# Kernel optimization log

Measured on AMD Instinct MI355X. Metric: run time of the kernel, lower is better.

The kernel has to match this reference:

```python
import jax, jax.numpy as jnp
import numpy as np

N_NODES = 50000
N_EDGES = 800000
IN_C, HID_C, OUT_C = 128, 128, 64
N_GRAPHS = 64
NEG_SLOPE = 0.2


def setup_inputs() -> dict:
    key = jax.random.key(0)
    ks = jax.random.split(key, 16)
    x = jax.random.normal(ks[0], (N_NODES, IN_C), dtype=jnp.float32)
    edge_index = jax.random.randint(ks[1], (2, N_EDGES), 0, N_NODES, dtype=jnp.int64)
    batch = jnp.sort(jax.random.randint(ks[2], (N_NODES,), 0, N_GRAPHS, dtype=jnp.int64))
    dims = [(IN_C, HID_C), (HID_C, HID_C), (HID_C, OUT_C)]
    inp = {"x": x, "edge_index": edge_index, "batch": batch}
    for l, (din, dout) in enumerate(dims):
        s = 1.0 / np.sqrt(din)
        inp[f"W{l}"] = jax.random.normal(ks[3 + 4 * l], (din, dout), dtype=jnp.float32) * s
        inp[f"as{l}"] = jax.random.normal(ks[4 + 4 * l], (dout,), dtype=jnp.float32) * 0.1
        inp[f"ad{l}"] = jax.random.normal(ks[5 + 4 * l], (dout,), dtype=jnp.float32) * 0.1
        inp[f"b{l}"] = jnp.zeros((dout,), dtype=jnp.float32)
    return inp


def gat_conv(x, src, dst, W, a_src, a_dst, b, n_nodes):
    # h: [N, dout]
    h = x @ W
    alpha_src = h @ a_src  # [N]
    alpha_dst = h @ a_dst  # [N]
    logits = jax.nn.leaky_relu(alpha_src[src] + alpha_dst[dst], NEG_SLOPE)  # [E]
    # segment softmax over incoming edges of each dst node
    m = jax.ops.segment_max(logits, dst, num_segments=n_nodes)
    e = jnp.exp(logits - m[dst])
    denom = jax.ops.segment_sum(e, dst, num_segments=n_nodes)
    alpha = e / denom[dst]  # [E]
    out = jax.ops.segment_sum(alpha[:, None] * h[src], dst, num_segments=n_nodes)
    return out + b


def reference(x, edge_index, batch, W0, as0, ad0, b0, W1, as1, ad1, b1, W2, as2, ad2, b2):
    n = x.shape[0]
    # add self loops (PyG GATConv default)
    loop = jnp.arange(n, dtype=edge_index.dtype)
    src = jnp.concatenate([edge_index[0], loop])
    dst = jnp.concatenate([edge_index[1], loop])
    h = jax.nn.relu(gat_conv(x, src, dst, W0, as0, ad0, b0, n))
    h = jax.nn.relu(gat_conv(h, src, dst, W1, as1, ad1, b1, n))
    h = gat_conv(h, src, dst, W2, as2, ad2, b2, n)
    # global_add_pool
    return jax.ops.segment_sum(h, batch, num_segments=N_GRAPHS)
```

## Files before the change

### kernel.cpp

```cpp
#include <hip/hip_runtime.h>
#include <hip/hip_fp16.h>
#include <math.h>

#define N_NODES 50000
#define N_EDGES 800000
#define N_GRAPHS 64
#define NEG_SLOPE 0.2f
#define SLOTS 64

#define BIN_NODES 256
#define NBINS 196
#define CAP 6144
#define P1_BLOCKS 192
#define BATCH 2048

typedef _Float16 f16x8 __attribute__((ext_vector_type(8)));
typedef float f32x4 __attribute__((ext_vector_type(4)));

__device__ __forceinline__ float leaky(float x) {
    return x > 0.f ? x : NEG_SLOPE * x;
}

struct __align__(16) half8 {
    __half2 h[4];
};

__global__ __launch_bounds__(256) void prep_kernel(const float* __restrict__ W0,
                                                   const float* __restrict__ W1,
                                                   const float* __restrict__ W2,
                                                   _Float16* __restrict__ Wt0,
                                                   _Float16* __restrict__ Wt1,
                                                   _Float16* __restrict__ Wt2,
                                                   unsigned int* __restrict__ bin_cursor,
                                                   float* __restrict__ dout, int osz) {
    const int t = blockIdx.x * 256 + threadIdx.x;
    if (t < NBINS) bin_cursor[t] = 0;
    if (t < osz) dout[t] = 0.f;
    const float* W;
    _Float16* Wt;
    int g, CTl, DOUTl;
    if (t < 2048) { W = W0; Wt = Wt0; g = t; CTl = 8; DOUTl = 128; }
    else if (t < 4096) { W = W1; Wt = Wt1; g = t - 2048; CTl = 8; DOUTl = 128; }
    else if (t < 5120) { W = W2; Wt = Wt2; g = t - 4096; CTl = 4; DOUTl = 64; }
    else return;
    const int kt = g / (CTl * 64);
    const int rem = g % (CTl * 64);
    const int ct = rem / 64;
    const int lane = rem % 64;
    const int kbase = kt * 32 + (lane >> 4) * 8;
    const int c = ct * 16 + (lane & 15);
#pragma unroll
    for (int b = 0; b < 8; ++b)
        Wt[(size_t)g * 8 + b] = (_Float16)W[(size_t)(kbase + b) * DOUTl + c];
}

template <int DOUT, typename XT>
__device__ __forceinline__ void mfma_gemm_body(const XT* __restrict__ X,
                                               const _Float16* __restrict__ Wt,
                                               const float* __restrict__ a_src,
                                               const float* __restrict__ a_dst,
                                               _Float16* __restrict__ H,
                                               float* __restrict__ as_,
                                               float* __restrict__ ad_, int N, int bid,
                                               _Float16* xs) {
    constexpr int CT = DOUT / 16;
    const int tid = threadIdx.x;
    const int n0 = bid * 64;

    if constexpr (sizeof(XT) == 4) {
        const float4* X4 = reinterpret_cast<const float4*>(X);
        for (int idx = tid; idx < 64 * 16; idx += 256) {
            const int r = idx >> 4, q = idx & 15;
            const int n = n0 + r;
            float4 v0 = make_float4(0.f, 0.f, 0.f, 0.f), v1 = v0;
            if (n < N) {
                v0 = X4[(size_t)n * 32 + 2 * q];
                v1 = X4[(size_t)n * 32 + 2 * q + 1];
            }
            f16x8 hv;
            hv[0] = (_Float16)v0.x; hv[1] = (_Float16)v0.y;
            hv[2] = (_Float16)v0.z; hv[3] = (_Float16)v0.w;
            hv[4] = (_Float16)v1.x; hv[5] = (_Float16)v1.y;
            hv[6] = (_Float16)v1.z; hv[7] = (_Float16)v1.w;
            *reinterpret_cast<f16x8*>(&xs[r * 128 + ((q ^ (r & 15)) << 3)]) = hv;
        }
    } else {
        const f16x8* X8 = reinterpret_cast<const f16x8*>(X);
        for (int idx = tid; idx < 64 * 16; idx += 256) {
            const int r = idx >> 4, q = idx & 15;
            const int n = n0 + r;
            f16x8 hv = {};
            if (n < N) hv = X8[(size_t)n * 16 + q];
            *reinterpret_cast<f16x8*>(&xs[r * 128 + ((q ^ (r & 15)) << 3)]) = hv;
        }
    }
    __syncthreads();

    const int wave = tid >> 6, lane = tid & 63;
    const int colb = lane & 15;
    const int kg = lane >> 4;
    const int arow = wave * 16 + colb;

    f32x4 acc[CT];
#pragma unroll
    for (int ct = 0; ct < CT; ++ct) {
        acc[ct][0] = 0.f; acc[ct][1] = 0.f; acc[ct][2] = 0.f; acc[ct][3] = 0.f;
    }
    const f16x8* Wt8 = reinterpret_cast<const f16x8*>(Wt);
#pragma unroll
    for (int kt = 0; kt < 4; ++kt) {
        f16x8 A = *reinterpret_cast<const f16x8*>(
            &xs[arow * 128 + (((kt * 4 + kg) ^ (arow & 15)) << 3)]);
#pragma unroll
        for (int ct = 0; ct < CT; ++ct) {
            f16x8 B = Wt8[(kt * CT + ct) * 64 + lane];
            acc[ct] = __builtin_amdgcn_mfma_f32_16x16x32_f16(A, B, acc[ct], 0, 0, 0);
        }
    }

    float ps[4] = {0.f, 0.f, 0.f, 0.f}, pd[4] = {0.f, 0.f, 0.f, 0.f};
#pragma unroll
    for (int ct = 0; ct < CT; ++ct) {
        const int col = ct * 16 + colb;
        const float asv = a_src[col];
        const float adv = a_dst[col];
#pragma unroll
        for (int r = 0; r < 4; ++r) {
            const float d = acc[ct][r];
            ps[r] += d * asv;
            pd[r] += d * adv;
            const int row = n0 + wave * 16 + kg * 4 + r;
            if (row < N) H[(size_t)row * DOUT + col] = (_Float16)d;
        }
    }
#pragma unroll
    for (int off = 1; off < 16; off <<= 1) {
#pragma unroll
        for (int r = 0; r < 4; ++r) {
            ps[r] += __shfl_xor(ps[r], off, 64);
            pd[r] += __shfl_xor(pd[r], off, 64);
        }
    }
    if (colb == 0) {
#pragma unroll
        for (int r = 0; r < 4; ++r) {
            const int row = n0 + wave * 16 + kg * 4 + r;
            if (row < N) {
                as_[row] = ps[r];
                ad_[row] = pd[r];
            }
        }
    }
}

template <int DOUT, typename XT>
__global__ __launch_bounds__(256) void mfma_gemm_kernel(const XT* __restrict__ X,
                                                        const _Float16* __restrict__ Wt,
                                                        const float* __restrict__ a_src,
                                                        const float* __restrict__ a_dst,
                                                        _Float16* __restrict__ H,
                                                        float* __restrict__ as_,
                                                        float* __restrict__ ad_, int N) {
    __shared__ __align__(16) _Float16 xs[64 * 128];
    mfma_gemm_body<DOUT, XT>(X, Wt, a_src, a_dst, H, as_, ad_, N, blockIdx.x, xs);
}

struct P1Smem {
    unsigned int stage[BATCH];
    int hist[NBINS];
    int off[NBINS];
    unsigned int gbase[NBINS];
    int total;
};

__device__ __forceinline__ void fill_pass1(const int* __restrict__ src,
                                           const int* __restrict__ dst,
                                           unsigned int* __restrict__ bin_cursor,
                                           unsigned int* __restrict__ bin_buf,
                                           int E, int bid, void* smem_raw) {
    P1Smem& S = *reinterpret_cast<P1Smem*>(smem_raw);
    const int tid = threadIdx.x;
    const int nbatch = (E + BATCH - 1) / BATCH;
    for (int b = bid; b < nbatch; b += P1_BLOCKS) {
        __syncthreads();
        for (int i = tid; i < NBINS; i += 256) S.hist[i] = 0;
        const int e0 = b * BATCH;
        unsigned int pk[8];
        int rk[8];
        bool ok[8];
#pragma unroll
        for (int k = 0; k < 8; ++k) {
            int e = e0 + tid + k * 256;
            ok[k] = (e < E);
            int d = ok[k] ? dst[e] : 0;
            int s = ok[k] ? src[e] : 0;
            pk[k] = ((unsigned)d << 16) | (unsigned)s;
            rk[k] = 0;
        }
        __syncthreads();
#pragma unroll
        for (int k = 0; k < 8; ++k)
            if (ok[k]) rk[k] = atomicAdd(&S.hist[pk[k] >> 24], 1);
        __syncthreads();
        for (int i = tid; i < NBINS; i += 256) S.off[i] = S.hist[i];
        __syncthreads();
#pragma unroll
        for (int d = 1; d < 256; d <<= 1) {
            int v = 0;
            if (tid < NBINS && tid >= d) v = S.off[tid - d];
            __syncthreads();
            if (tid < NBINS) S.off[tid] += v;
            __syncthreads();
        }
        if (tid == NBINS - 1) S.total = S.off[NBINS - 1];
        __syncthreads();
        if (tid < NBINS) S.off[tid] -= S.hist[tid];
        __syncthreads();
        if (tid < NBINS && S.hist[tid] > 0)
            S.gbase[tid] = atomicAdd(&bin_cursor[tid], (unsigned)S.hist[tid]);
#pragma unroll
        for (int k = 0; k < 8; ++k)
            if (ok[k]) S.stage[S.off[pk[k] >> 24] + rk[k]] = pk[k];
        __syncthreads();
        const int tot = S.total;
        for (int i = tid; i < tot; i += 256) {
            unsigned int v = S.stage[i];
            int bn = v >> 24;
            unsigned int p = S.gbase[bn] + (unsigned)(i - S.off[bn]);
            if (p < CAP) bin_buf[(size_t)bn * CAP + p] = v;
        }
    }
}

__global__ __launch_bounds__(256) void gemm0_fill_kernel(
    const float* __restrict__ X, const _Float16* __restrict__ Wt0,
    const float* __restrict__ a_src, const float* __restrict__ a_dst,
    _Float16* __restrict__ H, float* __restrict__ as_, float* __restrict__ ad_, int N,
    const int* __restrict__ src, const int* __restrict__ dst,
    unsigned int* __restrict__ bin_cursor, unsigned int* __restrict__ bin_buf, int E) {
    __shared__ __align__(16) unsigned char smem[16384];
    if (blockIdx.x < P1_BLOCKS) {
        fill_pass1(src, dst, bin_cursor, bin_buf, E, blockIdx.x, smem);
        return;
    }
    mfma_gemm_body<128, float>(X, Wt0, a_src, a_dst, H, as_, ad_, N, blockIdx.x - P1_BLOCKS,
                               reinterpret_cast<_Float16*>(smem));
}

__global__ __launch_bounds__(256) void fill_pass2(const unsigned int* __restrict__ bin_cursor,
                                                  const unsigned int* __restrict__ bin_buf,
                                                  int* __restrict__ cursor,
                                                  unsigned short* __restrict__ col, int N) {
    __shared__ unsigned short bk[BIN_NODES][SLOTS];
    __shared__ int cnt[BIN_NODES];
    const int b = blockIdx.x;
    const int tid = threadIdx.x;
    const int base = b * BIN_NODES;
    const int nn = min(BIN_NODES, N - base);
    if (nn <= 0) return;
    cnt[tid] = 0;
    __syncthreads();
    const int ec = min((int)bin_cursor[b], CAP);
    for (int i = tid; i < ec; i += 256) {
        unsigned int v = bin_buf[(size_t)b * CAP + i];
        int d = (int)(v >> 16) - base;
        int p = atomicAdd(&cnt[d], 1);
        if (p < SLOTS) bk[d][p] = (unsigned short)(v & 0xFFFFu);
    }
    __syncthreads();
    unsigned int* col32 = reinterpret_cast<unsigned int*>(col);
    const unsigned int* lds32 = reinterpret_cast<const unsigned int*>(&bk[0][0]);
    const int words = nn * (SLOTS / 2);
    for (int i = tid; i < words; i += 256)
        col32[(size_t)base * (SLOTS / 2) + i] = lds32[i];
    if (tid < nn) cursor[base + tid] = cnt[tid];
}

template <int DOUT, bool POOL>
__global__ __launch_bounds__(256) void gather_kernel(const half8* __restrict__ H8,
                                                     const float* __restrict__ as_,
                                                     const float* __restrict__ ad_,
                                                     const int* __restrict__ cursor,
                                                     const unsigned short* __restrict__ col,
                                                     const float* __restrict__ bias,
                                                     half8* __restrict__ OUT,
                                                     const int* __restrict__ batch,
                                                     float* __restrict__ pool_out, int N) {
    constexpr int NCH = DOUT / 8;
    constexpr int SUBS = 64 / NCH;
    __shared__ float pbuf[4][64];
    __shared__ int pg[4];
    const int wv = threadIdx.x >> 6;
    const int node = blockIdx.x * 4 + wv;
    if (!POOL && node >= N) return;
    const int l = threadIdx.x & 63;
    const int ch = l & (NCH - 1);
    const int sub = l / NCH;

    const float adn = ad_[node];
    const float sl = leaky(as_[node] + adn);
    const int rs = node << 6;
    const int re = rs + min(cursor[node], SLOTS);

    float acc[8] = {};
    float dsum = 0.f;

    int i = rs + sub;
    for (; i + 3 * SUBS < re; i += 4 * SUBS) {
        int s[4];
        float a[4];
        half8 h[4];
#pragma unroll
        for (int u = 0; u < 4; ++u) s[u] = col[i + u * SUBS];
#pragma unroll
        for (int u = 0; u < 4; ++u) a[u] = as_[s[u]];
#pragma unroll
        for (int u = 0; u < 4; ++u) h[u] = H8[(size_t)s[u] * NCH + ch];
#pragma unroll
        for (int u = 0; u < 4; ++u) {
            float ee = __expf(leaky(a[u] + adn));
#pragma unroll
            for (int j = 0; j < 4; ++j) {
                float2 f = __half22float2(h[u].h[j]);
                acc[2 * j] += ee * f.x;
                acc[2 * j + 1] += ee * f.y;
            }
            dsum += ee;
        }
    }
    for (; i + SUBS < re; i += 2 * SUBS) {
        int s0 = col[i], s1 = col[i + SUBS];
        float a0 = as_[s0], a1 = as_[s1];
        half8 h0 = H8[(size_t)s0 * NCH + ch];
        half8 h1 = H8[(size_t)s1 * NCH + ch];
        float e0 = __expf(leaky(a0 + adn));
        float e1 = __expf(leaky(a1 + adn));
#pragma unroll
        for (int j = 0; j < 4; ++j) {
            float2 f0 = __half22float2(h0.h[j]);
            float2 f1 = __half22float2(h1.h[j]);
            acc[2 * j] += e0 * f0.x + e1 * f1.x;
            acc[2 * j + 1] += e0 * f0.y + e1 * f1.y;
        }
        dsum += e0 + e1;
    }
    if (i < re) {
        int s0 = col[i];
        float e0 = __expf(leaky(as_[s0] + adn));
        half8 h0 = H8[(size_t)s0 * NCH + ch];
#pragma unroll
        for (int j = 0; j < 4; ++j) {
            float2 f = __half22float2(h0.h[j]);
            acc[2 * j] += e0 * f.x;
            acc[2 * j + 1] += e0 * f.y;
        }
        dsum += e0;
    }

#pragma unroll
    for (int off = 32; off >= NCH; off >>= 1)
        dsum += __shfl_xor(dsum, off, 64);
#pragma unroll
    for (int off = 32; off >= NCH; off >>= 1) {
#pragma unroll
        for (int j = 0; j < 8; ++j)
            acc[j] += __shfl_down(acc[j], off, 64);
    }

    if (l < NCH) {
        const float e_self = __expf(sl);
        half8 h = H8[(size_t)node * NCH + ch];
        const float inv_pre = dsum + e_self;
        const float inv = 1.f / inv_pre;
        const float4* b4 = reinterpret_cast<const float4*>(bias);
        const float4 ba = b4[2 * ch], bb = b4[2 * ch + 1];
        const float bj[8] = {ba.x, ba.y, ba.z, ba.w, bb.x, bb.y, bb.z, bb.w};
        float r[8];
#pragma unroll
        for (int j = 0; j < 4; ++j) {
            float2 f = __half22float2(h.h[j]);
            acc[2 * j] += e_self * f.x;
            acc[2 * j + 1] += e_self * f.y;
        }
#pragma unroll
        for (int j = 0; j < 8; ++j) {
            r[j] = acc[j] * inv + bj[j];
            if (!POOL) r[j] = fmaxf(r[j], 0.f);
        }
        if (POOL) {
#pragma unroll
            for (int j = 0; j < 8; ++j) pbuf[wv][ch * 8 + j] = r[j];
        } else {
            half8 o;
#pragma unroll
            for (int j = 0; j < 4; ++j)
                o.h[j] = __floats2half2_rn(r[2 * j], r[2 * j + 1]);
            OUT[(size_t)node * NCH + ch] = o;
        }
    }
    if (POOL) {
        if (l == 0) pg[wv] = batch[node];
        __syncthreads();
        if (threadIdx.x < 64) {
            const int c = threadIdx.x;
            const int g0 = pg[0], g3 = pg[3];
            if (g0 == g3) {
                atomicAdd(&pool_out[g0 * 64 + c],
                          pbuf[0][c] + pbuf[1][c] + pbuf[2][c] + pbuf[3][c]);
            } else {
#pragma unroll
                for (int w = 0; w < 4; ++w)
                    atomicAdd(&pool_out[pg[w] * 64 + c], pbuf[w][c]);
            }
        }
    }
}

extern "C" void kernel_launch(void* const* d_in, const int* in_sizes, int n_in,
                              void* d_out, int out_size, void* d_ws, size_t ws_size,
                              hipStream_t stream) {
    const float* x = (const float*)d_in[0];
    const int* edge_index = (const int*)d_in[1];
    const int* batch = (const int*)d_in[2];
    const float* W0 = (const float*)d_in[3];
    const float* as0 = (const float*)d_in[4];
    const float* ad0 = (const float*)d_in[5];
    const float* b0 = (const float*)d_in[6];
    const float* W1 = (const float*)d_in[7];
    const float* as1 = (const float*)d_in[8];
    const float* ad1 = (const float*)d_in[9];
    const float* b1 = (const float*)d_in[10];
    const float* W2 = (const float*)d_in[11];
    const float* as2 = (const float*)d_in[12];
    const float* ad2 = (const float*)d_in[13];
    const float* b2 = (const float*)d_in[14];

    const int* e_src = edge_index;
    const int* e_dst = edge_index + N_EDGES;

    char* p = (char*)d_ws;
    _Float16* X16 = (_Float16*)p;     p += (size_t)N_NODES * 128 * 2;
    _Float16* H = (_Float16*)p;       p += (size_t)N_NODES * 128 * 2;
    float* as_ = (float*)p;           p += (size_t)N_NODES * 4;
    float* ad_ = (float*)p;           p += (size_t)N_NODES * 4;
    int* cursor = (int*)p;            p += (size_t)N_NODES * 4;
    unsigned short* col = (unsigned short*)p; p += (size_t)N_NODES * SLOTS * 2;
    unsigned int* bin_cursor = (unsigned int*)p; p += (size_t)((NBINS + 3) & ~3) * 4;
    unsigned int* bin_buf = (unsigned int*)p; p += (size_t)NBINS * CAP * 4;
    _Float16* Wt0 = (_Float16*)p;     p += (size_t)16384 * 2;
    _Float16* Wt1 = (_Float16*)p;     p += (size_t)16384 * 2;
    _Float16* Wt2 = (_Float16*)p;     p += (size_t)8192 * 2;

    const int NODE_BLOCKS = (N_NODES + 3) / 4;
    const int GEMM_BLOCKS = (N_NODES + 63) / 64;

    prep_kernel<<<20, 256, 0, stream>>>(W0, W1, W2, Wt0, Wt1, Wt2, bin_cursor,
                                        (float*)d_out, out_size);

    gemm0_fill_kernel<<<P1_BLOCKS + GEMM_BLOCKS, 256, 0, stream>>>(
        x, Wt0, as0, ad0, H, as_, ad_, N_NODES, e_src, e_dst, bin_cursor, bin_buf, N_EDGES);
    fill_pass2<<<NBINS, 256, 0, stream>>>(bin_cursor, bin_buf, cursor, col, N_NODES);
    gather_kernel<128, false><<<NODE_BLOCKS, 256, 0, stream>>>(
        (const half8*)H, as_, ad_, cursor, col, b0, (half8*)X16, batch, nullptr, N_NODES);

    mfma_gemm_kernel<128, _Float16><<<GEMM_BLOCKS, 256, 0, stream>>>(
        X16, Wt1, as1, ad1, H, as_, ad_, N_NODES);
    gather_kernel<128, false><<<NODE_BLOCKS, 256, 0, stream>>>(
        (const half8*)H, as_, ad_, cursor, col, b1, (half8*)X16, batch, nullptr, N_NODES);

    mfma_gemm_kernel<64, _Float16><<<GEMM_BLOCKS, 256, 0, stream>>>(
        X16, Wt2, as2, ad2, H, as_, ad_, N_NODES);
    gather_kernel<64, true><<<NODE_BLOCKS, 256, 0, stream>>>(
        (const half8*)H, as_, ad_, cursor, col, b2, nullptr, batch, (float*)d_out, N_NODES);
}
```

Baseline: 250.8 us.

## Store H in 32-column slabs and split gather across column slices

The GEMM now writes H in a sliced layout of 32-channel slabs, one contiguous [N,32] array per slab, instead of row-major [N,DOUT]. The gather kernel becomes sgather_kernel: each block handles 4 nodes for one slab. Block indices are interleaved so that blocks sharing a slab run close together, which shrinks the gathered working set per slab and should raise L2 hit rates on random source-row reads. The cost is recomputing edge weights (exp) once per slab, with S times more blocks and col/as_ reads, and the launch relies on N_NODES being divisible by 4 because the node bounds check was removed.

```diff
diff --git a/kernel.cpp b/kernel.cpp
--- a/kernel.cpp
+++ b/kernel.cpp
@@ -20,10 +20,6 @@
 __device__ __forceinline__ float leaky(float x) {
     return x > 0.f ? x : NEG_SLOPE * x;
 }
-
-struct __align__(16) half8 {
-    __half2 h[4];
-};
 
 __global__ __launch_bounds__(256) void prep_kernel(const float* __restrict__ W0,
                                                    const float* __restrict__ W1,
@@ -59,7 +55,7 @@
                                                const _Float16* __restrict__ Wt,
                                                const float* __restrict__ a_src,
                                                const float* __restrict__ a_dst,
-                                               _Float16* __restrict__ H,
+                                               _Float16* __restrict__ Hs,
                                                float* __restrict__ as_,
                                                float* __restrict__ ad_, int N, int bid,
                                                _Float16* xs) {
@@ -124,13 +120,14 @@
         const int col = ct * 16 + colb;
         const float asv = a_src[col];
         const float adv = a_dst[col];
+        const size_t sbase = (size_t)(col >> 5) * N * 32 + (col & 31);
 #pragma unroll
         for (int r = 0; r < 4; ++r) {
             const float d = acc[ct][r];
             ps[r] += d * asv;
             pd[r] += d * adv;
             const int row = n0 + wave * 16 + kg * 4 + r;
-            if (row < N) H[(size_t)row * DOUT + col] = (_Float16)d;
+            if (row < N) Hs[sbase + (size_t)row * 32] = (_Float16)d;
         }
     }
 #pragma unroll
@@ -158,11 +155,11 @@
                                                         const _Float16* __restrict__ Wt,
                                                         const float* __restrict__ a_src,
                                                         const float* __restrict__ a_dst,
-                                                        _Float16* __restrict__ H,
+                                                        _Float16* __restrict__ Hs,
                                                         float* __restrict__ as_,
                                                         float* __restrict__ ad_, int N) {
     __shared__ __align__(16) _Float16 xs[64 * 128];
-    mfma_gemm_body<DOUT, XT>(X, Wt, a_src, a_dst, H, as_, ad_, N, blockIdx.x, xs);
+    mfma_gemm_body<DOUT, XT>(X, Wt, a_src, a_dst, Hs, as_, ad_, N, blockIdx.x, xs);
 }
 
 struct P1Smem {
@@ -235,7 +232,7 @@
 __global__ __launch_bounds__(256) void gemm0_fill_kernel(
     const float* __restrict__ X, const _Float16* __restrict__ Wt0,
     const float* __restrict__ a_src, const float* __restrict__ a_dst,
-    _Float16* __restrict__ H, float* __restrict__ as_, float* __restrict__ ad_, int N,
+    _Float16* __restrict__ Hs, float* __restrict__ as_, float* __restrict__ ad_, int N,
     const int* __restrict__ src, const int* __restrict__ dst,
     unsigned int* __restrict__ bin_cursor, unsigned int* __restrict__ bin_buf, int E) {
     __shared__ __align__(16) unsigned char smem[16384];
@@ -243,7 +240,7 @@
         fill_pass1(src, dst, bin_cursor, bin_buf, E, blockIdx.x, smem);
         return;
     }
-    mfma_gemm_body<128, float>(X, Wt0, a_src, a_dst, H, as_, ad_, N, blockIdx.x - P1_BLOCKS,
+    mfma_gemm_body<128, float>(X, Wt0, a_src, a_dst, Hs, as_, ad_, N, blockIdx.x - P1_BLOCKS,
                                reinterpret_cast<_Float16*>(smem));
 }
 
@@ -276,27 +273,29 @@
     if (tid < nn) cursor[base + tid] = cnt[tid];
 }
 
-template <int DOUT, bool POOL>
-__global__ __launch_bounds__(256) void gather_kernel(const half8* __restrict__ H8,
-                                                     const float* __restrict__ as_,
-                                                     const float* __restrict__ ad_,
-                                                     const int* __restrict__ cursor,
-                                                     const unsigned short* __restrict__ col,
-                                                     const float* __restrict__ bias,
-                                                     half8* __restrict__ OUT,
-                                                     const int* __restrict__ batch,
-                                                     float* __restrict__ pool_out, int N) {
-    constexpr int NCH = DOUT / 8;
-    constexpr int SUBS = 64 / NCH;
-    __shared__ float pbuf[4][64];
+template <int S, bool POOL>
+__global__ __launch_bounds__(256) void sgather_kernel(const _Float16* __restrict__ Hs,
+                                                      const float* __restrict__ as_,
+                                                      const float* __restrict__ ad_,
+                                                      const int* __restrict__ cursor,
+                                                      const unsigned short* __restrict__ col,
+                                                      const float* __restrict__ bias,
+                                                      _Float16* __restrict__ OUT,
+                                                      const int* __restrict__ batch,
+                                                      float* __restrict__ pool_out, int N) {
+    __shared__ float pbuf[4][32];
     __shared__ int pg[4];
+    const int j = blockIdx.x;
+    const int x = j & 7;
+    const int s = x & (S - 1);
+    const int g = (j >> 3) * (8 / S) + (x / S);
     const int wv = threadIdx.x >> 6;
-    const int node = blockIdx.x * 4 + wv;
-    if (!POOL && node >= N) return;
+    const int node = g * 4 + wv;
     const int l = threadIdx.x & 63;
-    const int ch = l & (NCH - 1);
-    const int sub = l / NCH;
-
+    const int ch4 = l & 3;
+    const int sub = l >> 2;
+
+    const _Float16* Hsl = Hs + (size_t)s * N * 32;
     const float adn = ad_[node];
     const float sl = leaky(as_[node] + adn);
     const int rs = node << 6;
@@ -304,113 +303,75 @@
 
     float acc[8] = {};
     float dsum = 0.f;
-
     int i = rs + sub;
-    for (; i + 3 * SUBS < re; i += 4 * SUBS) {
-        int s[4];
-        float a[4];
-        half8 h[4];
-#pragma unroll
-        for (int u = 0; u < 4; ++u) s[u] = col[i + u * SUBS];
-#pragma unroll
-        for (int u = 0; u < 4; ++u) a[u] = as_[s[u]];
-#pragma unroll
-        for (int u = 0; u < 4; ++u) h[u] = H8[(size_t)s[u] * NCH + ch];
-#pragma unroll
-        for (int u = 0; u < 4; ++u) {
-            float ee = __expf(leaky(a[u] + adn));
-#pragma unroll
-            for (int j = 0; j < 4; ++j) {
-                float2 f = __half22float2(h[u].h[j]);
-                acc[2 * j] += ee * f.x;
-                acc[2 * j + 1] += ee * f.y;
-            }
-            dsum += ee;
-        }
-    }
-    for (; i + SUBS < re; i += 2 * SUBS) {
-        int s0 = col[i], s1 = col[i + SUBS];
-        float a0 = as_[s0], a1 = as_[s1];
-        half8 h0 = H8[(size_t)s0 * NCH + ch];
-        half8 h1 = H8[(size_t)s1 * NCH + ch];
-        float e0 = __expf(leaky(a0 + adn));
-        float e1 = __expf(leaky(a1 + adn));
-#pragma unroll
-        for (int j = 0; j < 4; ++j) {
-            float2 f0 = __half22float2(h0.h[j]);
-            float2 f1 = __half22float2(h1.h[j]);
-            acc[2 * j] += e0 * f0.x + e1 * f1.x;
-            acc[2 * j + 1] += e0 * f0.y + e1 * f1.y;
-        }
+    for (; i + 16 < re; i += 32) {
+        int s0 = col[i];
+        int s1 = col[i + 16];
+        float e0 = __expf(leaky(as_[s0] + adn));
+        float e1 = __expf(leaky(as_[s1] + adn));
+        f16x8 h0 = *reinterpret_cast<const f16x8*>(&Hsl[(size_t)s0 * 32 + ch4 * 8]);
+        f16x8 h1 = *reinterpret_cast<const f16x8*>(&Hsl[(size_t)s1 * 32 + ch4 * 8]);
+#pragma unroll
+        for (int q = 0; q < 8; ++q)
+            acc[q] += e0 * (float)h0[q] + e1 * (float)h1[q];
         dsum += e0 + e1;
     }
     if (i < re) {
         int s0 = col[i];
         float e0 = __expf(leaky(as_[s0] + adn));
-        half8 h0 = H8[(size_t)s0 * NCH + ch];
-#pragma unroll
-        for (int j = 0; j < 4; ++j) {
-            float2 f = __half22float2(h0.h[j]);
-            acc[2 * j] += e0 * f.x;
-            acc[2 * j + 1] += e0 * f.y;
-        }
+        f16x8 h0 = *reinterpret_cast<const f16x8*>(&Hsl[(size_t)s0 * 32 + ch4 * 8]);
+#pragma unroll
+        for (int q = 0; q < 8; ++q)
+            acc[q] += e0 * (float)h0[q];
         dsum += e0;
     }
 
 #pragma unroll
-    for (int off = 32; off >= NCH; off >>= 1)
+    for (int off = 4; off <= 32; off <<= 1)
         dsum += __shfl_xor(dsum, off, 64);
 #pragma unroll
-    for (int off = 32; off >= NCH; off >>= 1) {
-#pragma unroll
-        for (int j = 0; j < 8; ++j)
-            acc[j] += __shfl_down(acc[j], off, 64);
-    }
-
-    if (l < NCH) {
+    for (int off = 32; off >= 4; off >>= 1) {
+#pragma unroll
+        for (int q = 0; q < 8; ++q)
+            acc[q] += __shfl_down(acc[q], off, 64);
+    }
+
+    if (l < 4) {
         const float e_self = __expf(sl);
-        half8 h = H8[(size_t)node * NCH + ch];
-        const float inv_pre = dsum + e_self;
-        const float inv = 1.f / inv_pre;
-        const float4* b4 = reinterpret_cast<const float4*>(bias);
-        const float4 ba = b4[2 * ch], bb = b4[2 * ch + 1];
+        f16x8 hself = *reinterpret_cast<const f16x8*>(&Hsl[(size_t)node * 32 + ch4 * 8]);
+        const float inv = 1.f / (dsum + e_self);
+        const float4* b4 = reinterpret_cast<const float4*>(bias + s * 32);
+        const float4 ba = b4[2 * ch4], bb = b4[2 * ch4 + 1];
         const float bj[8] = {ba.x, ba.y, ba.z, ba.w, bb.x, bb.y, bb.z, bb.w};
         float r[8];
 #pragma unroll
-        for (int j = 0; j < 4; ++j) {
-            float2 f = __half22float2(h.h[j]);
-            acc[2 * j] += e_self * f.x;
-            acc[2 * j + 1] += e_self * f.y;
-        }
-#pragma unroll
-        for (int j = 0; j < 8; ++j) {
-            r[j] = acc[j] * inv + bj[j];
-            if (!POOL) r[j] = fmaxf(r[j], 0.f);
+        for (int q = 0; q < 8; ++q) {
+            r[q] = (acc[q] + e_self * (float)hself[q]) * inv + bj[q];
+            if (!POOL) r[q] = fmaxf(r[q], 0.f);
         }
         if (POOL) {
 #pragma unroll
-            for (int j = 0; j < 8; ++j) pbuf[wv][ch * 8 + j] = r[j];
+            for (int q = 0; q < 8; ++q) pbuf[wv][ch4 * 8 + q] = r[q];
         } else {
-            half8 o;
-#pragma unroll
-            for (int j = 0; j < 4; ++j)
-                o.h[j] = __floats2half2_rn(r[2 * j], r[2 * j + 1]);
-            OUT[(size_t)node * NCH + ch] = o;
+            f16x8 o;
+#pragma unroll
+            for (int q = 0; q < 8; ++q) o[q] = (_Float16)r[q];
+            *reinterpret_cast<f16x8*>(&OUT[(size_t)node * 128 + s * 32 + ch4 * 8]) = o;
         }
     }
     if (POOL) {
         if (l == 0) pg[wv] = batch[node];
         __syncthreads();
-        if (threadIdx.x < 64) {
+        if (threadIdx.x < 32) {
             const int c = threadIdx.x;
             const int g0 = pg[0], g3 = pg[3];
             if (g0 == g3) {
-                atomicAdd(&pool_out[g0 * 64 + c],
+                atomicAdd(&pool_out[g0 * 64 + s * 32 + c],
                           pbuf[0][c] + pbuf[1][c] + pbuf[2][c] + pbuf[3][c]);
             } else {
 #pragma unroll
                 for (int w = 0; w < 4; ++w)
-                    atomicAdd(&pool_out[pg[w] * 64 + c], pbuf[w][c]);
+                    atomicAdd(&pool_out[pg[w] * 64 + s * 32 + c], pbuf[w][c]);
             }
         }
     }
@@ -440,7 +401,7 @@
 
     char* p = (char*)d_ws;
     _Float16* X16 = (_Float16*)p;     p += (size_t)N_NODES * 128 * 2;
-    _Float16* H = (_Float16*)p;       p += (size_t)N_NODES * 128 * 2;
+    _Float16* Hs = (_Float16*)p;      p += (size_t)N_NODES * 128 * 2;
     float* as_ = (float*)p;           p += (size_t)N_NODES * 4;
     float* ad_ = (float*)p;           p += (size_t)N_NODES * 4;
     int* cursor = (int*)p;            p += (size_t)N_NODES * 4;
@@ -451,25 +412,26 @@
     _Float16* Wt1 = (_Float16*)p;     p += (size_t)16384 * 2;
     _Float16* Wt2 = (_Float16*)p;     p += (size_t)8192 * 2;
 
-    const int NODE_BLOCKS = (N_NODES + 3) / 4;
     const int GEMM_BLOCKS = (N_NODES + 63) / 64;
+    const int SG4_BLOCKS = (N_NODES / 4) * 4;
+    const int SG2_BLOCKS = (N_NODES / 4) * 2;
 
     prep_kernel<<<20, 256, 0, stream>>>(W0, W1, W2, Wt0, Wt1, Wt2, bin_cursor,
                                         (float*)d_out, out_size);
 
     gemm0_fill_kernel<<<P1_BLOCKS + GEMM_BLOCKS, 256, 0, stream>>>(
-        x, Wt0, as0, ad0, H, as_, ad_, N_NODES, e_src, e_dst, bin_cursor, bin_buf, N_EDGES);
+        x, Wt0, as0, ad0, Hs, as_, ad_, N_NODES, e_src, e_dst, bin_cursor, bin_buf, N_EDGES);
     fill_pass2<<<NBINS, 256, 0, stream>>>(bin_cursor, bin_buf, cursor, col, N_NODES);
-    gather_kernel<128, false><<<NODE_BLOCKS, 256, 0, stream>>>(
-        (const half8*)H, as_, ad_, cursor, col, b0, (half8*)X16, batch, nullptr, N_NODES);
+    sgather_kernel<4, false><<<SG4_BLOCKS, 256, 0, stream>>>(
+        Hs, as_, ad_, cursor, col, b0, X16, batch, nullptr, N_NODES);
 
     mfma_gemm_kernel<128, _Float16><<<GEMM_BLOCKS, 256, 0, stream>>>(
-        X16, Wt1, as1, ad1, H, as_, ad_, N_NODES);
-    gather_kernel<128, false><<<NODE_BLOCKS, 256, 0, stream>>>(
-        (const half8*)H, as_, ad_, cursor, col, b1, (half8*)X16, batch, nullptr, N_NODES);
+        X16, Wt1, as1, ad1, Hs, as_, ad_, N_NODES);
+    sgather_kernel<4, false><<<SG4_BLOCKS, 256, 0, stream>>>(
+        Hs, as_, ad_, cursor, col, b1, X16, batch, nullptr, N_NODES);
 
     mfma_gemm_kernel<64, _Float16><<<GEMM_BLOCKS, 256, 0, stream>>>(
-        X16, Wt2, as2, ad2, H, as_, ad_, N_NODES);
-    gather_kernel<64, true><<<NODE_BLOCKS, 256, 0, stream>>>(
-        (const half8*)H, as_, ad_, cursor, col, b2, nullptr, batch, (float*)d_out, N_NODES);
-}
+        X16, Wt2, as2, ad2, Hs, as_, ad_, N_NODES);
+    sgather_kernel<2, true><<<SG2_BLOCKS, 256, 0, stream>>>(
+        Hs, as_, ad_, cursor, col, b2, nullptr, batch, (float*)d_out, N_NODES);
+}
```

New measurement: 362.5 us. 1.45x slower.
